# Performance work log

Hardware: AMD Instinct MI355X
Metric: run time of the kernel (lower is better)

Reference implementation:

```python
import jax, jax.numpy as jnp
import numpy as np

NIN = 1024
NOUT = 1024
NHEADS = 16
DHEAD = NOUT // NHEADS


def setup_inputs() -> dict:
    key = jax.random.key(0)
    k1, k2, k3, k4 = jax.random.split(key, 4)
    y = jax.random.normal(k1, (2, 2048, NIN), dtype=jnp.float32)
    Wqkv = jax.random.normal(k2, (NIN, 3 * NOUT), dtype=jnp.float32) * (1.0 / np.sqrt(NIN))
    Wff = jax.random.normal(k3, (NOUT, NOUT), dtype=jnp.float32) * (1.0 / np.sqrt(NOUT))
    bff = jax.random.normal(k4, (NOUT,), dtype=jnp.float32) * 0.01
    return {"y": y, "Wqkv": Wqkv, "Wff": Wff, "bff": bff}


def reference(y, Wqkv, Wff, bff):
    b, n, _ = y.shape
    qkv = y @ Wqkv  # [b, n, 3*nout]
    qkv = qkv.reshape(b, n, 3, NHEADS, DHEAD).transpose(2, 0, 3, 1, 4)
    q, k, v = qkv[0], qkv[1], qkv[2]  # each [b, h, n, d]
    att = jnp.einsum('bhqd,bhkd->bhqk', q, k)
    causal = jnp.triu(jnp.ones((n, n), dtype=bool), k=1)
    att = jnp.where(causal, -jnp.inf, att)
    att = jax.nn.softmax(att / jnp.sqrt(jnp.float32(DHEAD)), axis=-1)
    ctx = jnp.einsum('bhqk,bhkd->bhqd', att, v)
    ctx = ctx.transpose(0, 2, 1, 3).reshape(b, n, NOUT)
    return ctx @ Wff + bff
```

## Files before the change

kernel.cpp:

```cpp
#include <hip/hip_runtime.h>
#include <stdint.h>

#define NHEADS 16
#define DHEAD 64
#define SEQ 2048
#define BATCH 2
#define NINF 1024
#define NOUTF 1024
#define N3 3072
#define MTOT 4096

typedef unsigned short US;
typedef __attribute__((ext_vector_type(8))) short short8;
typedef __attribute__((ext_vector_type(4))) short short4v;
typedef __attribute__((ext_vector_type(4))) float f32x4;

__device__ inline US f2bf(float f) {
  union { float f; unsigned u; } v; v.f = f;
  unsigned r = v.u + 0x7fffu + ((v.u >> 16) & 1u);
  return (US)(r >> 16);
}

__device__ inline f32x4 mfma16(short8 a, short8 b, f32x4 c) {
  return __builtin_amdgcn_mfma_f32_16x16x32_bf16(a, b, c, 0, 0, 0);
}

__device__ inline f32x4 mfma16k16(short4v a, short4v b, f32x4 c) {
  return __builtin_amdgcn_mfma_f32_16x16x16bf16_1k(a, b, c, 0, 0, 0);
}

__device__ inline void async16(const US* g, US* l) {
  __builtin_amdgcn_global_load_lds(
      (const __attribute__((address_space(1))) unsigned int*)g,
      (__attribute__((address_space(3))) unsigned int*)l, 16, 0, 0);
}

__global__ __launch_bounds__(256) void k_pre(
    const float* __restrict__ y, US* __restrict__ ybf,
    const float* __restrict__ Wqkv, const float* __restrict__ Wff,
    US* __restrict__ dq, US* __restrict__ df) {
  __shared__ float tile[32][33];
  int bl = blockIdx.x;
  int tid = threadIdx.x;
  if (bl < 4096) {
    int i = bl * 256 + tid;
    float4 v = ((const float4*)y)[i];
    ushort4 o;
    o.x = f2bf(v.x); o.y = f2bf(v.y); o.z = f2bf(v.z); o.w = f2bf(v.w);
    ((ushort4*)ybf)[i] = o;
  } else {
    int bl2 = bl - 4096;
    int bxi = bl2 & 127, byi = bl2 >> 7;
    const float* src; US* dst; int C;
    if (bxi < 96) { src = Wqkv; dst = dq; C = N3; }
    else          { src = Wff;  dst = df; C = NOUTF; bxi -= 96; }
    int bx = bxi * 32, by = byi * 32;
    int tx = tid & 31, ty = tid >> 5;
    for (int i = 0; i < 32; i += 8)
      tile[ty + i][tx] = src[(size_t)(by + ty + i) * C + bx + tx];
    __syncthreads();
    for (int i = 0; i < 32; i += 8)
      dst[(size_t)(bx + ty + i) * 1024 + by + tx] = f2bf(tile[tx][ty + i]);
  }
}

__global__ void k_vtrans(const US* __restrict__ src, US* __restrict__ dst) {
  __shared__ US tile[32][33];
  int bh = blockIdx.z;
  int bx = blockIdx.x * 32;
  int by = blockIdx.y * 32;
  int tx = threadIdx.x, ty = threadIdx.y;
  const US* s0 = src + (size_t)bh * SEQ * DHEAD;
  US* d0 = dst + (size_t)bh * DHEAD * SEQ;
  for (int i = 0; i < 32; i += 8)
    tile[ty + i][tx] = s0[(size_t)(by + ty + i) * DHEAD + bx + tx];
  __syncthreads();
  for (int i = 0; i < 32; i += 8)
    d0[(size_t)(bx + ty + i) * SEQ + by + tx] = tile[tx][ty + i];
}

__global__ __launch_bounds__(256) void k_gemm_qkv(
    const US* __restrict__ A,
    const US* __restrict__ Bt,
    US* __restrict__ qbuf, US* __restrict__ kbuf, US* __restrict__ vbuf) {
  __shared__ US As[128 * 32];
  __shared__ US Bs[128 * 32];
  int tid = threadIdx.x;
  int wave = tid >> 6, lane = tid & 63, lm = lane & 15, lk = lane >> 4;
  int wm = wave >> 1, wn = wave & 1;
  int mbase = blockIdx.y * 128, nbase = blockIdx.x * 128;

  f32x4 acc[4][4];
#pragma unroll
  for (int i = 0; i < 4; ++i)
#pragma unroll
    for (int j = 0; j < 4; ++j) acc[i][j] = (f32x4){0.f, 0.f, 0.f, 0.f};

  const US* ga = A + (size_t)(mbase + (tid >> 2)) * NINF + (tid & 3) * 8;
  const US* gb = Bt + (size_t)(nbase + (tid >> 2)) * NINF + (tid & 3) * 8;
  US* la = As + tid * 8;
  US* lb = Bs + tid * 8;

  for (int kt = 0; kt < NINF / 32; ++kt) {
    int ko = kt * 32;
    async16(ga + ko, la);
    async16(ga + ko + (size_t)64 * NINF, la + 64 * 32);
    async16(gb + ko, lb);
    async16(gb + ko + (size_t)64 * NINF, lb + 64 * 32);
    __syncthreads();
    short8 a[4], b[4];
#pragma unroll
    for (int i = 0; i < 4; ++i)
      a[i] = *(const short8*)(As + (wm * 64 + i * 16 + lm) * 32 + lk * 8);
#pragma unroll
    for (int j = 0; j < 4; ++j)
      b[j] = *(const short8*)(Bs + (wn * 64 + j * 16 + lm) * 32 + lk * 8);
#pragma unroll
    for (int i = 0; i < 4; ++i)
#pragma unroll
      for (int j = 0; j < 4; ++j) acc[i][j] = mfma16(b[j], a[i], acc[i][j]);
    __syncthreads();
  }

  int which = nbase >> 10;
  US* dsts = (which == 0) ? qbuf : (which == 1) ? kbuf : vbuf;
  float sc = (which == 0) ? 0.18033688011112042f : 1.f;
  int hh = ((nbase + wn * 64) & 1023) >> 6;
#pragma unroll
  for (int i = 0; i < 4; ++i) {
    int row = mbase + wm * 64 + i * 16 + lm;
    int bh = (row >> 11) * NHEADS + hh;
    int s = row & (SEQ - 1);
    US* base = dsts + ((size_t)bh * SEQ + s) * DHEAD;
#pragma unroll
    for (int j = 0; j < 4; ++j) {
      int d0 = j * 16 + lk * 4;
      uint32_t lo = (uint32_t)f2bf(acc[i][j][0] * sc) | ((uint32_t)f2bf(acc[i][j][1] * sc) << 16);
      uint32_t hi = (uint32_t)f2bf(acc[i][j][2] * sc) | ((uint32_t)f2bf(acc[i][j][3] * sc) << 16);
      uint2 pv; pv.x = lo; pv.y = hi;
      *(uint2*)(base + d0) = pv;
    }
  }
}

__global__ __launch_bounds__(256) void k_attn(
    const US* __restrict__ qbuf, const US* __restrict__ kbuf,
    const US* __restrict__ vtbuf, US* __restrict__ ctx) {
  __shared__ US Ks[2][64 * 64];
  __shared__ US Vs[2][64 * 64];
  int tid = threadIdx.x;
  int w = tid >> 6, lane = tid & 63;
  int lm = lane & 15, lk = lane >> 4;
  int bl = blockIdx.x;
  int xcd = bl & 7, g = bl >> 3;
  int bh = (g & 3) * 8 + xcd;
  int q4 = g >> 2;
  int rnd = q4 >> 3, qq = q4 & 7;
  int s = (rnd == 0) ? 31 - qq : (rnd == 1) ? qq : (rnd == 2) ? 23 - qq : 8 + qq;
  int qb = s * 64 + w * 16;
  int nt = s + 1;

  const US* kbase = kbuf + (size_t)bh * SEQ * DHEAD;
  const US* vtb = vtbuf + (size_t)bh * DHEAD * SEQ;
  const US* qr = qbuf + ((size_t)bh * SEQ + qb + lm) * DHEAD + lk * 8;
  short8 qf0 = *(const short8*)(qr);
  short8 qf1 = *(const short8*)(qr + 32);

  int swz = ((lane & 7) ^ (lane >> 3)) * 8;
  const US* gsrc[4];
  US* ldst[4];
  int step[4];
#pragma unroll
  for (int j = 0; j < 4; ++j) {
    int u = w + 4 * j;
    if (u < 8) {
      gsrc[j] = kbase + (size_t)(u * 8 + (lane >> 3)) * DHEAD + swz;
      ldst[j] = &Ks[0][0] + u * 512 + lane * 8;
      step[j] = 64 * DHEAD;
    } else {
      int i = u - 8;
      gsrc[j] = vtb + (size_t)(i * 8 + (lane >> 3)) * SEQ + swz;
      ldst[j] = &Vs[0][0] + i * 512 + lane * 8;
      step[j] = 64;
    }
  }

  int xorv = lm & 7;
  int ck0 = ((lk) ^ xorv) * 16;
  int ck1 = ((4 + lk) ^ xorv) * 16;
  int cv[4];
#pragma unroll
  for (int kg = 0; kg < 4; ++kg)
    cv[kg] = (((kg * 2 + (lk >> 1)) ^ xorv) * 16) + (lk & 1) * 8;

  f32x4 o[4];
#pragma unroll
  for (int dg = 0; dg < 4; ++dg) o[dg] = (f32x4){0.f, 0.f, 0.f, 0.f};
  f32x4 lacc = (f32x4){0.f, 0.f, 0.f, 0.f};
  const short4v kones = {(short)0x3F80, (short)0x3F80, (short)0x3F80, (short)0x3F80};

  auto body = [&](const char* Kc, const char* Vc, int kg, bool dm) {
    const char* kr = Kc + (kg * 16 + lm) * 128;
    short8 ka0 = *(const short8*)(kr + ck0);
    short8 ka1 = *(const short8*)(kr + ck1);
    f32x4 st = (f32x4){0.f, 0.f, 0.f, 0.f};
    st = mfma16(ka0, qf0, st);
    st = mfma16(ka1, qf1, st);
    uint32_t ue[4];
#pragma unroll
    for (int r = 0; r < 4; ++r) {
      float v = st[r];
      if (dm && (lk * 4 + r > lm)) v = -INFINITY;
      union { float f; uint32_t u; } cv2;
      cv2.f = exp2f(v);
      ue[r] = cv2.u + 0x8000u;
    }
    union { short4v s4; uint32_t u[2]; } pk;
    pk.u[0] = __builtin_amdgcn_perm(ue[1], ue[0], 0x07060302u);
    pk.u[1] = __builtin_amdgcn_perm(ue[3], ue[2], 0x07060302u);
    lacc = mfma16k16(kones, pk.s4, lacc);
    const char* vr = Vc + lm * 128 + cv[kg];
#pragma unroll
    for (int dg = 0; dg < 4; ++dg) {
      short4v va = *(const short4v*)(vr + dg * 2048);
      o[dg] = mfma16k16(va, pk.s4, o[dg]);
    }
  };

#pragma unroll
  for (int j = 0; j < 4; ++j) { async16(gsrc[j], ldst[j]); gsrc[j] += step[j]; }
  if (nt > 1) {
#pragma unroll
    for (int j = 0; j < 4; ++j) { async16(gsrc[j], ldst[j] + 4096); gsrc[j] += step[j]; }
  }

  for (int t = 0; t < nt; ++t) {
    if (t + 1 < nt) asm volatile("s_waitcnt vmcnt(4)" ::: "memory");
    else            asm volatile("s_waitcnt vmcnt(0)" ::: "memory");
    __builtin_amdgcn_s_barrier();
    asm volatile("" ::: "memory");
    const char* Kc = (const char*)Ks + (t & 1) * 8192;
    const char* Vc = (const char*)Vs + (t & 1) * 8192;
    if (t < s) {
#pragma unroll
      for (int kg = 0; kg < 4; ++kg) body(Kc, Vc, kg, false);
    } else {
      for (int kg = 0; kg < w; ++kg) body(Kc, Vc, kg, false);
      body(Kc, Vc, w, true);
    }
    asm volatile("" ::: "memory");
    __builtin_amdgcn_s_barrier();
    asm volatile("" ::: "memory");
    if (t + 2 < nt) {
#pragma unroll
      for (int j = 0; j < 4; ++j) {
        async16(gsrc[j], ldst[j] + (t & 1) * 4096);
        gsrc[j] += step[j];
      }
    }
  }

  float inv = 1.f / lacc[0];

  US* crow = ctx + ((size_t)(bh >> 4) * SEQ + qb + lm) * NOUTF + (bh & 15) * DHEAD;
#pragma unroll
  for (int dg = 0; dg < 4; ++dg) {
    union { short4v s4; uint32_t u[2]; } pk;
    pk.u[0] = (uint32_t)f2bf(o[dg][0] * inv) | ((uint32_t)f2bf(o[dg][1] * inv) << 16);
    pk.u[1] = (uint32_t)f2bf(o[dg][2] * inv) | ((uint32_t)f2bf(o[dg][3] * inv) << 16);
    *(short4v*)(crow + dg * 16 + lk * 4) = pk.s4;
  }
}

__global__ __launch_bounds__(256) void k_gemm_out(
    const US* __restrict__ A, const US* __restrict__ Bt,
    const float* __restrict__ bias, float* __restrict__ out) {
  __shared__ US As[64 * 32];
  __shared__ US Bs[64 * 32];
  int tid = threadIdx.x;
  int wave = tid >> 6, lane = tid & 63, lm = lane & 15, lk = lane >> 4;
  int wm = wave >> 1, wn = wave & 1;
  int mbase = blockIdx.y * 64, nbase = blockIdx.x * 64;

  f32x4 acc[2][2];
#pragma unroll
  for (int i = 0; i < 2; ++i)
#pragma unroll
    for (int j = 0; j < 2; ++j) acc[i][j] = (f32x4){0.f, 0.f, 0.f, 0.f};

  const US* ga = A + (size_t)(mbase + (tid >> 2)) * NOUTF + (tid & 3) * 8;
  const US* gb = Bt + (size_t)(nbase + (tid >> 2)) * NOUTF + (tid & 3) * 8;
  US* la = As + tid * 8;
  US* lb = Bs + tid * 8;

  for (int kt = 0; kt < NOUTF / 32; ++kt) {
    int ko = kt * 32;
    async16(ga + ko, la);
    async16(gb + ko, lb);
    __syncthreads();
    short8 a[2], b[2];
#pragma unroll
    for (int i = 0; i < 2; ++i)
      a[i] = *(const short8*)(As + (wm * 32 + i * 16 + lm) * 32 + lk * 8);
#pragma unroll
    for (int j = 0; j < 2; ++j)
      b[j] = *(const short8*)(Bs + (wn * 32 + j * 16 + lm) * 32 + lk * 8);
#pragma unroll
    for (int i = 0; i < 2; ++i)
#pragma unroll
      for (int j = 0; j < 2; ++j) acc[i][j] = mfma16(b[j], a[i], acc[i][j]);
    __syncthreads();
  }

#pragma unroll
  for (int j = 0; j < 2; ++j) {
    int n0 = nbase + wn * 32 + j * 16 + lk * 4;
    float4 bv = *(const float4*)(bias + n0);
#pragma unroll
    for (int i = 0; i < 2; ++i) {
      int row = mbase + wm * 32 + i * 16 + lm;
      float4 ov;
      ov.x = acc[i][j][0] + bv.x;
      ov.y = acc[i][j][1] + bv.y;
      ov.z = acc[i][j][2] + bv.z;
      ov.w = acc[i][j][3] + bv.w;
      *(float4*)(out + (size_t)row * NOUTF + n0) = ov;
    }
  }
}

extern "C" void kernel_launch(void* const* d_in, const int* in_sizes, int n_in,
                              void* d_out, int out_size, void* d_ws, size_t ws_size,
                              hipStream_t stream) {
  const float* y    = (const float*)d_in[0];
  const float* Wqkv = (const float*)d_in[1];
  const float* Wff  = (const float*)d_in[2];
  const float* bff  = (const float*)d_in[3];
  float* out = (float*)d_out;

  char* ws = (char*)d_ws;
  US* ybf   = (US*)(ws);
  US* ctx   = (US*)(ws);
  US* wqkvt = (US*)(ws + (8u << 20));
  US* wfft  = (US*)(ws + (14u << 20));
  US* qbuf  = (US*)(ws + (16u << 20));
  US* kbuf  = (US*)(ws + (24u << 20));
  US* vbuf  = (US*)(ws + (32u << 20));
  US* vtbuf = (US*)(ws + (40u << 20));

  k_pre<<<dim3(8192), 256, 0, stream>>>(y, ybf, Wqkv, Wff, wqkvt, wfft);
  k_gemm_qkv<<<dim3(N3 / 128, MTOT / 128), 256, 0, stream>>>(ybf, wqkvt, qbuf, kbuf, vbuf);
  k_vtrans<<<dim3(DHEAD / 32, SEQ / 32, BATCH * NHEADS), dim3(32, 8), 0, stream>>>(vbuf, vtbuf);
  k_attn<<<dim3(1024), 256, 0, stream>>>(qbuf, kbuf, vtbuf, ctx);
  k_gemm_out<<<dim3(NOUTF / 64, MTOT / 64), 256, 0, stream>>>(ctx, wfft, bff, out);
}
```

Measured before the change: 183.0 us.

## Deepen QKV GEMM K-tile with XOR-swizzled LDS and enlarge output GEMM tile

The QKV GEMM now stages a 64-wide K slice per iteration instead of 32, halving the barrier count, and places the data with an XOR swizzle on 16-byte chunks to avoid LDS bank conflicts. The output GEMM moves from 64x64 to 128x64 block tiles, with each wave covering 32 rows and all 64 columns, and swaps the MFMA operand order so its epilogue writes scalar floats along columns. The larger tiles raise data reuse per LDS load but double shared memory and accumulator registers, which can lower occupancy. The new scalar stores in the output epilogue may also be less efficient than the earlier float4 stores.

```diff
diff --git a/kernel.cpp b/kernel.cpp
--- a/kernel.cpp
+++ b/kernel.cpp
@@ -83,8 +83,8 @@
     const US* __restrict__ A,
     const US* __restrict__ Bt,
     US* __restrict__ qbuf, US* __restrict__ kbuf, US* __restrict__ vbuf) {
-  __shared__ US As[128 * 32];
-  __shared__ US Bs[128 * 32];
+  __shared__ US As[128 * 64];
+  __shared__ US Bs[128 * 64];
   int tid = threadIdx.x;
   int wave = tid >> 6, lane = tid & 63, lm = lane & 15, lk = lane >> 4;
   int wm = wave >> 1, wn = wave & 1;
@@ -96,29 +96,41 @@
 #pragma unroll
     for (int j = 0; j < 4; ++j) acc[i][j] = (f32x4){0.f, 0.f, 0.f, 0.f};
 
-  const US* ga = A + (size_t)(mbase + (tid >> 2)) * NINF + (tid & 3) * 8;
-  const US* gb = Bt + (size_t)(nbase + (tid >> 2)) * NINF + (tid & 3) * 8;
+  int ru = tid >> 3;
+  int su = (tid & 7) ^ (ru & 7);
+  const US* ga = A + (size_t)(mbase + ru) * NINF + su * 8;
+  const US* gb = Bt + (size_t)(nbase + ru) * NINF + su * 8;
   US* la = As + tid * 8;
   US* lb = Bs + tid * 8;
 
-  for (int kt = 0; kt < NINF / 32; ++kt) {
-    int ko = kt * 32;
-    async16(ga + ko, la);
-    async16(ga + ko + (size_t)64 * NINF, la + 64 * 32);
-    async16(gb + ko, lb);
-    async16(gb + ko + (size_t)64 * NINF, lb + 64 * 32);
-    __syncthreads();
-    short8 a[4], b[4];
-#pragma unroll
-    for (int i = 0; i < 4; ++i)
-      a[i] = *(const short8*)(As + (wm * 64 + i * 16 + lm) * 32 + lk * 8);
-#pragma unroll
-    for (int j = 0; j < 4; ++j)
-      b[j] = *(const short8*)(Bs + (wn * 64 + j * 16 + lm) * 32 + lk * 8);
-#pragma unroll
-    for (int i = 0; i < 4; ++i)
-#pragma unroll
-      for (int j = 0; j < 4; ++j) acc[i][j] = mfma16(b[j], a[i], acc[i][j]);
+  int xorv = lm & 7;
+
+  for (int kt = 0; kt < 16; ++kt) {
+    int ko = kt * 64;
+#pragma unroll
+    for (int p = 0; p < 4; ++p) {
+      async16(ga + ko + (size_t)(p * 32) * NINF, la + p * 2048);
+      async16(gb + ko + (size_t)(p * 32) * NINF, lb + p * 2048);
+    }
+    __syncthreads();
+    short8 a[2][4], b[2][4];
+#pragma unroll
+    for (int kk = 0; kk < 2; ++kk) {
+      int u = (kk * 4 + lk) ^ xorv;
+#pragma unroll
+      for (int i = 0; i < 4; ++i)
+        a[kk][i] = *(const short8*)(As + (wm * 64 + i * 16 + lm) * 64 + u * 8);
+#pragma unroll
+      for (int j = 0; j < 4; ++j)
+        b[kk][j] = *(const short8*)(Bs + (wn * 64 + j * 16 + lm) * 64 + u * 8);
+    }
+#pragma unroll
+    for (int kk = 0; kk < 2; ++kk)
+#pragma unroll
+      for (int i = 0; i < 4; ++i)
+#pragma unroll
+        for (int j = 0; j < 4; ++j)
+          acc[i][j] = mfma16(b[kk][j], a[kk][i], acc[i][j]);
     __syncthreads();
   }
 
@@ -275,18 +287,17 @@
 __global__ __launch_bounds__(256) void k_gemm_out(
     const US* __restrict__ A, const US* __restrict__ Bt,
     const float* __restrict__ bias, float* __restrict__ out) {
-  __shared__ US As[64 * 32];
+  __shared__ US As[128 * 32];
   __shared__ US Bs[64 * 32];
   int tid = threadIdx.x;
   int wave = tid >> 6, lane = tid & 63, lm = lane & 15, lk = lane >> 4;
-  int wm = wave >> 1, wn = wave & 1;
-  int mbase = blockIdx.y * 64, nbase = blockIdx.x * 64;
-
-  f32x4 acc[2][2];
+  int mbase = blockIdx.y * 128, nbase = blockIdx.x * 64;
+
+  f32x4 acc[2][4];
 #pragma unroll
   for (int i = 0; i < 2; ++i)
 #pragma unroll
-    for (int j = 0; j < 2; ++j) acc[i][j] = (f32x4){0.f, 0.f, 0.f, 0.f};
+    for (int j = 0; j < 4; ++j) acc[i][j] = (f32x4){0.f, 0.f, 0.f, 0.f};
 
   const US* ga = A + (size_t)(mbase + (tid >> 2)) * NOUTF + (tid & 3) * 8;
   const US* gb = Bt + (size_t)(nbase + (tid >> 2)) * NOUTF + (tid & 3) * 8;
@@ -296,36 +307,34 @@
   for (int kt = 0; kt < NOUTF / 32; ++kt) {
     int ko = kt * 32;
     async16(ga + ko, la);
+    async16(ga + ko + (size_t)64 * NOUTF, la + 64 * 32);
     async16(gb + ko, lb);
     __syncthreads();
-    short8 a[2], b[2];
+    short8 a[2], b[4];
 #pragma unroll
     for (int i = 0; i < 2; ++i)
-      a[i] = *(const short8*)(As + (wm * 32 + i * 16 + lm) * 32 + lk * 8);
-#pragma unroll
-    for (int j = 0; j < 2; ++j)
-      b[j] = *(const short8*)(Bs + (wn * 32 + j * 16 + lm) * 32 + lk * 8);
+      a[i] = *(const short8*)(As + (wave * 32 + i * 16 + lm) * 32 + lk * 8);
+#pragma unroll
+    for (int j = 0; j < 4; ++j)
+      b[j] = *(const short8*)(Bs + (j * 16 + lm) * 32 + lk * 8);
 #pragma unroll
     for (int i = 0; i < 2; ++i)
 #pragma unroll
-      for (int j = 0; j < 2; ++j) acc[i][j] = mfma16(b[j], a[i], acc[i][j]);
-    __syncthreads();
-  }
-
-#pragma unroll
-  for (int j = 0; j < 2; ++j) {
-    int n0 = nbase + wn * 32 + j * 16 + lk * 4;
-    float4 bv = *(const float4*)(bias + n0);
-#pragma unroll
-    for (int i = 0; i < 2; ++i) {
-      int row = mbase + wm * 32 + i * 16 + lm;
-      float4 ov;
-      ov.x = acc[i][j][0] + bv.x;
-      ov.y = acc[i][j][1] + bv.y;
-      ov.z = acc[i][j][2] + bv.z;
-      ov.w = acc[i][j][3] + bv.w;
-      *(float4*)(out + (size_t)row * NOUTF + n0) = ov;
-    }
+      for (int j = 0; j < 4; ++j) acc[i][j] = mfma16(a[i], b[j], acc[i][j]);
+    __syncthreads();
+  }
+
+#pragma unroll
+  for (int j = 0; j < 4; ++j) {
+    int col = nbase + j * 16 + lm;
+    float bv = bias[col];
+#pragma unroll
+    for (int i = 0; i < 2; ++i)
+#pragma unroll
+      for (int r = 0; r < 4; ++r) {
+        int row = mbase + wave * 32 + i * 16 + lk * 4 + r;
+        out[(size_t)row * NOUTF + col] = acc[i][j][r] + bv;
+      }
   }
 }
 
@@ -352,5 +361,5 @@
   k_gemm_qkv<<<dim3(N3 / 128, MTOT / 128), 256, 0, stream>>>(ybf, wqkvt, qbuf, kbuf, vbuf);
   k_vtrans<<<dim3(DHEAD / 32, SEQ / 32, BATCH * NHEADS), dim3(32, 8), 0, stream>>>(vbuf, vtbuf);
   k_attn<<<dim3(1024), 256, 0, stream>>>(qbuf, kbuf, vtbuf, ctx);
-  k_gemm_out<<<dim3(NOUTF / 64, MTOT / 64), 256, 0, stream>>>(ctx, wfft, bff, out);
-}
+  k_gemm_out<<<dim3(NOUTF / 64, MTOT / 128), 256, 0, stream>>>(ctx, wfft, bff, out);
+}
```

Measured after the change: 194.1 us. +6.1%, slower.

## Fuse all stages into one persistent kernel with software grid barriers

Applied to the files above, without the earlier changes.

Replaces the five separate kernel launches with a single persistent kernel of 1024 blocks. The stages (convert/transpose, QKV GEMM, V transpose, attention, output GEMM) are separated by atomic-counter grid barriers, and the counter lives in the first word of the output buffer, zeroed by a memset. The aim is to remove kernel launch gaps and tail idling between stages. In exchange, correctness depends on all 1024 blocks being co-resident (launch bounds 256,4). The QKV GEMM also uses only 768 of the blocks, and the spin barriers add their own overhead.

```diff
diff --git a/kernel.cpp b/kernel.cpp
--- a/kernel.cpp
+++ b/kernel.cpp
@@ -9,6 +9,7 @@
 #define NOUTF 1024
 #define N3 3072
 #define MTOT 4096
+#define MB (1u << 20)
 
 typedef unsigned short US;
 typedef __attribute__((ext_vector_type(8))) short short8;
@@ -35,296 +36,320 @@
       (__attribute__((address_space(3))) unsigned int*)l, 16, 0, 0);
 }
 
-__global__ __launch_bounds__(256) void k_pre(
-    const float* __restrict__ y, US* __restrict__ ybf,
-    const float* __restrict__ Wqkv, const float* __restrict__ Wff,
-    US* __restrict__ dq, US* __restrict__ df) {
-  __shared__ float tile[32][33];
+__device__ inline void gbar(unsigned* cnt, unsigned th) {
+  __syncthreads();
+  if (threadIdx.x == 0) {
+    __threadfence();
+    atomicAdd(cnt, 1u);
+    while (__hip_atomic_load(cnt, __ATOMIC_RELAXED, __HIP_MEMORY_SCOPE_AGENT) < th)
+      __builtin_amdgcn_s_sleep(2);
+    __threadfence();
+  }
+  __syncthreads();
+}
+
+__global__ __launch_bounds__(256, 4) void k_fused(
+    const float* __restrict__ y, const float* __restrict__ Wqkv,
+    const float* __restrict__ Wff, const float* __restrict__ bff,
+    float* __restrict__ out, char* __restrict__ ws) {
+  __shared__ __align__(16) char smem[32768];
+  US* ybf   = (US*)(ws);
+  US* ctx   = (US*)(ws);
+  US* wqkvt = (US*)(ws + 8 * MB);
+  US* wfft  = (US*)(ws + 14 * MB);
+  US* qbuf  = (US*)(ws + 16 * MB);
+  US* kbuf  = (US*)(ws + 24 * MB);
+  US* vbuf  = (US*)(ws + 32 * MB);
+  US* vtbuf = (US*)(ws + 40 * MB);
+  unsigned* cnt = (unsigned*)out;
   int bl = blockIdx.x;
   int tid = threadIdx.x;
-  if (bl < 4096) {
-    int i = bl * 256 + tid;
-    float4 v = ((const float4*)y)[i];
-    ushort4 o;
-    o.x = f2bf(v.x); o.y = f2bf(v.y); o.z = f2bf(v.z); o.w = f2bf(v.w);
-    ((ushort4*)ybf)[i] = o;
-  } else {
-    int bl2 = bl - 4096;
-    int bxi = bl2 & 127, byi = bl2 >> 7;
-    const float* src; US* dst; int C;
-    if (bxi < 96) { src = Wqkv; dst = dq; C = N3; }
-    else          { src = Wff;  dst = df; C = NOUTF; bxi -= 96; }
-    int bx = bxi * 32, by = byi * 32;
+  int wave = tid >> 6, lane = tid & 63, lm = lane & 15, lk = lane >> 4;
+
+  {
+#pragma unroll
+    for (int p = 0; p < 4; ++p) {
+      int i = (p * 1024 + bl) * 256 + tid;
+      float4 v = ((const float4*)y)[i];
+      ushort4 o;
+      o.x = f2bf(v.x); o.y = f2bf(v.y); o.z = f2bf(v.z); o.w = f2bf(v.w);
+      ((ushort4*)ybf)[i] = o;
+    }
+    float (*tile)[33] = (float(*)[33])smem;
     int tx = tid & 31, ty = tid >> 5;
-    for (int i = 0; i < 32; i += 8)
-      tile[ty + i][tx] = src[(size_t)(by + ty + i) * C + bx + tx];
-    __syncthreads();
-    for (int i = 0; i < 32; i += 8)
-      dst[(size_t)(bx + ty + i) * 1024 + by + tx] = f2bf(tile[tx][ty + i]);
-  }
-}
-
-__global__ void k_vtrans(const US* __restrict__ src, US* __restrict__ dst) {
-  __shared__ US tile[32][33];
-  int bh = blockIdx.z;
-  int bx = blockIdx.x * 32;
-  int by = blockIdx.y * 32;
-  int tx = threadIdx.x, ty = threadIdx.y;
-  const US* s0 = src + (size_t)bh * SEQ * DHEAD;
-  US* d0 = dst + (size_t)bh * DHEAD * SEQ;
-  for (int i = 0; i < 32; i += 8)
-    tile[ty + i][tx] = s0[(size_t)(by + ty + i) * DHEAD + bx + tx];
-  __syncthreads();
-  for (int i = 0; i < 32; i += 8)
-    d0[(size_t)(bx + ty + i) * SEQ + by + tx] = tile[tx][ty + i];
-}
-
-__global__ __launch_bounds__(256) void k_gemm_qkv(
-    const US* __restrict__ A,
-    const US* __restrict__ Bt,
-    US* __restrict__ qbuf, US* __restrict__ kbuf, US* __restrict__ vbuf) {
-  __shared__ US As[128 * 32];
-  __shared__ US Bs[128 * 32];
-  int tid = threadIdx.x;
-  int wave = tid >> 6, lane = tid & 63, lm = lane & 15, lk = lane >> 4;
-  int wm = wave >> 1, wn = wave & 1;
-  int mbase = blockIdx.y * 128, nbase = blockIdx.x * 128;
-
-  f32x4 acc[4][4];
-#pragma unroll
-  for (int i = 0; i < 4; ++i)
-#pragma unroll
-    for (int j = 0; j < 4; ++j) acc[i][j] = (f32x4){0.f, 0.f, 0.f, 0.f};
-
-  const US* ga = A + (size_t)(mbase + (tid >> 2)) * NINF + (tid & 3) * 8;
-  const US* gb = Bt + (size_t)(nbase + (tid >> 2)) * NINF + (tid & 3) * 8;
-  US* la = As + tid * 8;
-  US* lb = Bs + tid * 8;
-
-  for (int kt = 0; kt < NINF / 32; ++kt) {
-    int ko = kt * 32;
-    async16(ga + ko, la);
-    async16(ga + ko + (size_t)64 * NINF, la + 64 * 32);
-    async16(gb + ko, lb);
-    async16(gb + ko + (size_t)64 * NINF, lb + 64 * 32);
-    __syncthreads();
-    short8 a[4], b[4];
+    for (int q = 0; q < 4; ++q) {
+      int t = bl * 4 + q;
+      int bxi = t & 127, byi = t >> 7;
+      const float* src; US* dst; int C;
+      if (bxi < 96) { src = Wqkv; dst = wqkvt; C = N3; }
+      else          { src = Wff;  dst = wfft;  C = NOUTF; bxi -= 96; }
+      int bx = bxi * 32, by = byi * 32;
+      for (int i2 = 0; i2 < 32; i2 += 8)
+        tile[ty + i2][tx] = src[(size_t)(by + ty + i2) * C + bx + tx];
+      __syncthreads();
+      for (int i2 = 0; i2 < 32; i2 += 8)
+        dst[(size_t)(bx + ty + i2) * 1024 + by + tx] = f2bf(tile[tx][ty + i2]);
+      __syncthreads();
+    }
+  }
+  gbar(cnt, 1024u);
+
+  if (bl < 768) {
+    US* As = (US*)smem;
+    US* Bs = (US*)(smem + 8192);
+    int wm = wave >> 1, wn = wave & 1;
+    int mbase = (bl / 24) * 128, nbase = (bl % 24) * 128;
+
+    f32x4 acc[4][4];
 #pragma unroll
     for (int i = 0; i < 4; ++i)
-      a[i] = *(const short8*)(As + (wm * 64 + i * 16 + lm) * 32 + lk * 8);
-#pragma unroll
-    for (int j = 0; j < 4; ++j)
-      b[j] = *(const short8*)(Bs + (wn * 64 + j * 16 + lm) * 32 + lk * 8);
-#pragma unroll
-    for (int i = 0; i < 4; ++i)
-#pragma unroll
-      for (int j = 0; j < 4; ++j) acc[i][j] = mfma16(b[j], a[i], acc[i][j]);
-    __syncthreads();
-  }
-
-  int which = nbase >> 10;
-  US* dsts = (which == 0) ? qbuf : (which == 1) ? kbuf : vbuf;
-  float sc = (which == 0) ? 0.18033688011112042f : 1.f;
-  int hh = ((nbase + wn * 64) & 1023) >> 6;
-#pragma unroll
-  for (int i = 0; i < 4; ++i) {
-    int row = mbase + wm * 64 + i * 16 + lm;
-    int bh = (row >> 11) * NHEADS + hh;
-    int s = row & (SEQ - 1);
-    US* base = dsts + ((size_t)bh * SEQ + s) * DHEAD;
+#pragma unroll
+      for (int j = 0; j < 4; ++j) acc[i][j] = (f32x4){0.f, 0.f, 0.f, 0.f};
+
+    const US* ga = ybf + (size_t)(mbase + (tid >> 2)) * NINF + (tid & 3) * 8;
+    const US* gb = wqkvt + (size_t)(nbase + (tid >> 2)) * NINF + (tid & 3) * 8;
+    US* la = As + tid * 8;
+    US* lb = Bs + tid * 8;
+
+    for (int kt = 0; kt < 32; ++kt) {
+      int ko = kt * 32;
+      async16(ga + ko, la);
+      async16(ga + ko + (size_t)64 * NINF, la + 2048);
+      async16(gb + ko, lb);
+      async16(gb + ko + (size_t)64 * NINF, lb + 2048);
+      __syncthreads();
+      short8 a[4], b[4];
+#pragma unroll
+      for (int i = 0; i < 4; ++i)
+        a[i] = *(const short8*)(As + (wm * 64 + i * 16 + lm) * 32 + lk * 8);
+#pragma unroll
+      for (int j = 0; j < 4; ++j)
+        b[j] = *(const short8*)(Bs + (wn * 64 + j * 16 + lm) * 32 + lk * 8);
+#pragma unroll
+      for (int i = 0; i < 4; ++i)
+#pragma unroll
+        for (int j = 0; j < 4; ++j) acc[i][j] = mfma16(b[j], a[i], acc[i][j]);
+      __syncthreads();
+    }
+
+    int which = nbase >> 10;
+    US* dsts = (which == 0) ? qbuf : (which == 1) ? kbuf : vbuf;
+    float sc = (which == 0) ? 0.18033688011112042f : 1.f;
+    int hh = ((nbase + wn * 64) & 1023) >> 6;
+#pragma unroll
+    for (int i = 0; i < 4; ++i) {
+      int row = mbase + wm * 64 + i * 16 + lm;
+      int bh = (row >> 11) * NHEADS + hh;
+      int s = row & (SEQ - 1);
+      US* base = dsts + ((size_t)bh * SEQ + s) * DHEAD;
+#pragma unroll
+      for (int j = 0; j < 4; ++j) {
+        int d0 = j * 16 + lk * 4;
+        uint32_t lo = (uint32_t)f2bf(acc[i][j][0] * sc) | ((uint32_t)f2bf(acc[i][j][1] * sc) << 16);
+        uint32_t hi = (uint32_t)f2bf(acc[i][j][2] * sc) | ((uint32_t)f2bf(acc[i][j][3] * sc) << 16);
+        uint2 pv; pv.x = lo; pv.y = hi;
+        *(uint2*)(base + d0) = pv;
+      }
+    }
+  }
+  gbar(cnt, 2048u);
+
+  {
+    US (*tile)[33] = (US(*)[33])smem;
+    int tx = tid & 31, ty = tid >> 5;
+#pragma unroll
+    for (int q = 0; q < 4; ++q) {
+      int t = q * 1024 + bl;
+      int bh = t & 31;
+      int sy = (t >> 5) & 63;
+      int dx = t >> 11;
+      const US* s0 = vbuf + (size_t)bh * SEQ * DHEAD;
+      US* d0 = vtbuf + (size_t)bh * DHEAD * SEQ;
+      int bx = dx * 32, by = sy * 32;
+      for (int i2 = 0; i2 < 32; i2 += 8)
+        tile[ty + i2][tx] = s0[(size_t)(by + ty + i2) * DHEAD + bx + tx];
+      __syncthreads();
+      for (int i2 = 0; i2 < 32; i2 += 8)
+        d0[(size_t)(bx + ty + i2) * SEQ + by + tx] = tile[tx][ty + i2];
+      __syncthreads();
+    }
+  }
+  gbar(cnt, 3072u);
+
+  {
+    US* KsP = (US*)smem;
+    US* VsP = (US*)(smem + 16384);
+    int w = wave;
+    int xcd = bl & 7, g = bl >> 3;
+    int bh = (g & 3) * 8 + xcd;
+    int q4 = g >> 2;
+    int rnd = q4 >> 3, qq = q4 & 7;
+    int s = (rnd == 0) ? 31 - qq : (rnd == 1) ? qq : (rnd == 2) ? 23 - qq : 8 + qq;
+    int qb = s * 64 + w * 16;
+    int nt = s + 1;
+
+    const US* kbase = kbuf + (size_t)bh * SEQ * DHEAD;
+    const US* vtb = vtbuf + (size_t)bh * DHEAD * SEQ;
+    const US* qr = qbuf + ((size_t)bh * SEQ + qb + lm) * DHEAD + lk * 8;
+    short8 qf0 = *(const short8*)(qr);
+    short8 qf1 = *(const short8*)(qr + 32);
+
+    int swz = ((lane & 7) ^ (lane >> 3)) * 8;
+    const US* gsrc[4];
+    US* ldst[4];
+    int step[4];
 #pragma unroll
     for (int j = 0; j < 4; ++j) {
-      int d0 = j * 16 + lk * 4;
-      uint32_t lo = (uint32_t)f2bf(acc[i][j][0] * sc) | ((uint32_t)f2bf(acc[i][j][1] * sc) << 16);
-      uint32_t hi = (uint32_t)f2bf(acc[i][j][2] * sc) | ((uint32_t)f2bf(acc[i][j][3] * sc) << 16);
-      uint2 pv; pv.x = lo; pv.y = hi;
-      *(uint2*)(base + d0) = pv;
-    }
-  }
-}
-
-__global__ __launch_bounds__(256) void k_attn(
-    const US* __restrict__ qbuf, const US* __restrict__ kbuf,
-    const US* __restrict__ vtbuf, US* __restrict__ ctx) {
-  __shared__ US Ks[2][64 * 64];
-  __shared__ US Vs[2][64 * 64];
-  int tid = threadIdx.x;
-  int w = tid >> 6, lane = tid & 63;
-  int lm = lane & 15, lk = lane >> 4;
-  int bl = blockIdx.x;
-  int xcd = bl & 7, g = bl >> 3;
-  int bh = (g & 3) * 8 + xcd;
-  int q4 = g >> 2;
-  int rnd = q4 >> 3, qq = q4 & 7;
-  int s = (rnd == 0) ? 31 - qq : (rnd == 1) ? qq : (rnd == 2) ? 23 - qq : 8 + qq;
-  int qb = s * 64 + w * 16;
-  int nt = s + 1;
-
-  const US* kbase = kbuf + (size_t)bh * SEQ * DHEAD;
-  const US* vtb = vtbuf + (size_t)bh * DHEAD * SEQ;
-  const US* qr = qbuf + ((size_t)bh * SEQ + qb + lm) * DHEAD + lk * 8;
-  short8 qf0 = *(const short8*)(qr);
-  short8 qf1 = *(const short8*)(qr + 32);
-
-  int swz = ((lane & 7) ^ (lane >> 3)) * 8;
-  const US* gsrc[4];
-  US* ldst[4];
-  int step[4];
-#pragma unroll
-  for (int j = 0; j < 4; ++j) {
-    int u = w + 4 * j;
-    if (u < 8) {
-      gsrc[j] = kbase + (size_t)(u * 8 + (lane >> 3)) * DHEAD + swz;
-      ldst[j] = &Ks[0][0] + u * 512 + lane * 8;
-      step[j] = 64 * DHEAD;
-    } else {
-      int i = u - 8;
-      gsrc[j] = vtb + (size_t)(i * 8 + (lane >> 3)) * SEQ + swz;
-      ldst[j] = &Vs[0][0] + i * 512 + lane * 8;
-      step[j] = 64;
-    }
-  }
-
-  int xorv = lm & 7;
-  int ck0 = ((lk) ^ xorv) * 16;
-  int ck1 = ((4 + lk) ^ xorv) * 16;
-  int cv[4];
-#pragma unroll
-  for (int kg = 0; kg < 4; ++kg)
-    cv[kg] = (((kg * 2 + (lk >> 1)) ^ xorv) * 16) + (lk & 1) * 8;
-
-  f32x4 o[4];
-#pragma unroll
-  for (int dg = 0; dg < 4; ++dg) o[dg] = (f32x4){0.f, 0.f, 0.f, 0.f};
-  f32x4 lacc = (f32x4){0.f, 0.f, 0.f, 0.f};
-  const short4v kones = {(short)0x3F80, (short)0x3F80, (short)0x3F80, (short)0x3F80};
-
-  auto body = [&](const char* Kc, const char* Vc, int kg, bool dm) {
-    const char* kr = Kc + (kg * 16 + lm) * 128;
-    short8 ka0 = *(const short8*)(kr + ck0);
-    short8 ka1 = *(const short8*)(kr + ck1);
-    f32x4 st = (f32x4){0.f, 0.f, 0.f, 0.f};
-    st = mfma16(ka0, qf0, st);
-    st = mfma16(ka1, qf1, st);
-    uint32_t ue[4];
-#pragma unroll
-    for (int r = 0; r < 4; ++r) {
-      float v = st[r];
-      if (dm && (lk * 4 + r > lm)) v = -INFINITY;
-      union { float f; uint32_t u; } cv2;
-      cv2.f = exp2f(v);
-      ue[r] = cv2.u + 0x8000u;
-    }
-    union { short4v s4; uint32_t u[2]; } pk;
-    pk.u[0] = __builtin_amdgcn_perm(ue[1], ue[0], 0x07060302u);
-    pk.u[1] = __builtin_amdgcn_perm(ue[3], ue[2], 0x07060302u);
-    lacc = mfma16k16(kones, pk.s4, lacc);
-    const char* vr = Vc + lm * 128 + cv[kg];
+      int u = w + 4 * j;
+      if (u < 8) {
+        gsrc[j] = kbase + (size_t)(u * 8 + (lane >> 3)) * DHEAD + swz;
+        ldst[j] = KsP + u * 512 + lane * 8;
+        step[j] = 64 * DHEAD;
+      } else {
+        int i = u - 8;
+        gsrc[j] = vtb + (size_t)(i * 8 + (lane >> 3)) * SEQ + swz;
+        ldst[j] = VsP + i * 512 + lane * 8;
+        step[j] = 64;
+      }
+    }
+
+    int xorv = lm & 7;
+    int ck0 = ((lk) ^ xorv) * 16;
+    int ck1 = ((4 + lk) ^ xorv) * 16;
+    int cv[4];
+#pragma unroll
+    for (int kg = 0; kg < 4; ++kg)
+      cv[kg] = (((kg * 2 + (lk >> 1)) ^ xorv) * 16) + (lk & 1) * 8;
+
+    f32x4 o[4];
+#pragma unroll
+    for (int dg = 0; dg < 4; ++dg) o[dg] = (f32x4){0.f, 0.f, 0.f, 0.f};
+    f32x4 lacc = (f32x4){0.f, 0.f, 0.f, 0.f};
+    const short4v kones = {(short)0x3F80, (short)0x3F80, (short)0x3F80, (short)0x3F80};
+
+    auto body = [&](const char* Kc, const char* Vc, int kg, bool dm) {
+      const char* kr = Kc + (kg * 16 + lm) * 128;
+      short8 ka0 = *(const short8*)(kr + ck0);
+      short8 ka1 = *(const short8*)(kr + ck1);
+      f32x4 st = (f32x4){0.f, 0.f, 0.f, 0.f};
+      st = mfma16(ka0, qf0, st);
+      st = mfma16(ka1, qf1, st);
+      uint32_t ue[4];
+#pragma unroll
+      for (int r = 0; r < 4; ++r) {
+        float v = st[r];
+        if (dm && (lk * 4 + r > lm)) v = -INFINITY;
+        union { float f; uint32_t u; } cv2;
+        cv2.f = exp2f(v);
+        ue[r] = cv2.u + 0x8000u;
+      }
+      union { short4v s4; uint32_t u[2]; } pk;
+      pk.u[0] = __builtin_amdgcn_perm(ue[1], ue[0], 0x07060302u);
+      pk.u[1] = __builtin_amdgcn_perm(ue[3], ue[2], 0x07060302u);
+      lacc = mfma16k16(kones, pk.s4, lacc);
+      const char* vr = Vc + lm * 128 + cv[kg];
+#pragma unroll
+      for (int dg = 0; dg < 4; ++dg) {
+        short4v va = *(const short4v*)(vr + dg * 2048);
+        o[dg] = mfma16k16(va, pk.s4, o[dg]);
+      }
+    };
+
+#pragma unroll
+    for (int j = 0; j < 4; ++j) { async16(gsrc[j], ldst[j]); gsrc[j] += step[j]; }
+    if (nt > 1) {
+#pragma unroll
+      for (int j = 0; j < 4; ++j) { async16(gsrc[j], ldst[j] + 4096); gsrc[j] += step[j]; }
+    }
+
+    for (int t = 0; t < nt; ++t) {
+      if (t + 1 < nt) asm volatile("s_waitcnt vmcnt(4)" ::: "memory");
+      else            asm volatile("s_waitcnt vmcnt(0)" ::: "memory");
+      __builtin_amdgcn_s_barrier();
+      asm volatile("" ::: "memory");
+      const char* Kc = (const char*)KsP + (t & 1) * 8192;
+      const char* Vc = (const char*)VsP + (t & 1) * 8192;
+      if (t < s) {
+#pragma unroll
+        for (int kg = 0; kg < 4; ++kg) body(Kc, Vc, kg, false);
+      } else {
+        for (int kg = 0; kg < w; ++kg) body(Kc, Vc, kg, false);
+        body(Kc, Vc, w, true);
+      }
+      asm volatile("" ::: "memory");
+      __builtin_amdgcn_s_barrier();
+      asm volatile("" ::: "memory");
+      if (t + 2 < nt) {
+#pragma unroll
+        for (int j = 0; j < 4; ++j) {
+          async16(gsrc[j], ldst[j] + (t & 1) * 4096);
+          gsrc[j] += step[j];
+        }
+      }
+    }
+
+    float inv = 1.f / lacc[0];
+    US* crow = ctx + ((size_t)(bh >> 4) * SEQ + qb + lm) * NOUTF + (bh & 15) * DHEAD;
 #pragma unroll
     for (int dg = 0; dg < 4; ++dg) {
-      short4v va = *(const short4v*)(vr + dg * 2048);
-      o[dg] = mfma16k16(va, pk.s4, o[dg]);
-    }
-  };
-
-#pragma unroll
-  for (int j = 0; j < 4; ++j) { async16(gsrc[j], ldst[j]); gsrc[j] += step[j]; }
-  if (nt > 1) {
-#pragma unroll
-    for (int j = 0; j < 4; ++j) { async16(gsrc[j], ldst[j] + 4096); gsrc[j] += step[j]; }
-  }
-
-  for (int t = 0; t < nt; ++t) {
-    if (t + 1 < nt) asm volatile("s_waitcnt vmcnt(4)" ::: "memory");
-    else            asm volatile("s_waitcnt vmcnt(0)" ::: "memory");
-    __builtin_amdgcn_s_barrier();
-    asm volatile("" ::: "memory");
-    const char* Kc = (const char*)Ks + (t & 1) * 8192;
-    const char* Vc = (const char*)Vs + (t & 1) * 8192;
-    if (t < s) {
-#pragma unroll
-      for (int kg = 0; kg < 4; ++kg) body(Kc, Vc, kg, false);
-    } else {
-      for (int kg = 0; kg < w; ++kg) body(Kc, Vc, kg, false);
-      body(Kc, Vc, w, true);
-    }
-    asm volatile("" ::: "memory");
-    __builtin_amdgcn_s_barrier();
-    asm volatile("" ::: "memory");
-    if (t + 2 < nt) {
-#pragma unroll
-      for (int j = 0; j < 4; ++j) {
-        async16(gsrc[j], ldst[j] + (t & 1) * 4096);
-        gsrc[j] += step[j];
-      }
-    }
-  }
-
-  float inv = 1.f / lacc[0];
-
-  US* crow = ctx + ((size_t)(bh >> 4) * SEQ + qb + lm) * NOUTF + (bh & 15) * DHEAD;
-#pragma unroll
-  for (int dg = 0; dg < 4; ++dg) {
-    union { short4v s4; uint32_t u[2]; } pk;
-    pk.u[0] = (uint32_t)f2bf(o[dg][0] * inv) | ((uint32_t)f2bf(o[dg][1] * inv) << 16);
-    pk.u[1] = (uint32_t)f2bf(o[dg][2] * inv) | ((uint32_t)f2bf(o[dg][3] * inv) << 16);
-    *(short4v*)(crow + dg * 16 + lk * 4) = pk.s4;
-  }
-}
-
-__global__ __launch_bounds__(256) void k_gemm_out(
-    const US* __restrict__ A, const US* __restrict__ Bt,
-    const float* __restrict__ bias, float* __restrict__ out) {
-  __shared__ US As[64 * 32];
-  __shared__ US Bs[64 * 32];
-  int tid = threadIdx.x;
-  int wave = tid >> 6, lane = tid & 63, lm = lane & 15, lk = lane >> 4;
-  int wm = wave >> 1, wn = wave & 1;
-  int mbase = blockIdx.y * 64, nbase = blockIdx.x * 64;
-
-  f32x4 acc[2][2];
-#pragma unroll
-  for (int i = 0; i < 2; ++i)
-#pragma unroll
-    for (int j = 0; j < 2; ++j) acc[i][j] = (f32x4){0.f, 0.f, 0.f, 0.f};
-
-  const US* ga = A + (size_t)(mbase + (tid >> 2)) * NOUTF + (tid & 3) * 8;
-  const US* gb = Bt + (size_t)(nbase + (tid >> 2)) * NOUTF + (tid & 3) * 8;
-  US* la = As + tid * 8;
-  US* lb = Bs + tid * 8;
-
-  for (int kt = 0; kt < NOUTF / 32; ++kt) {
-    int ko = kt * 32;
-    async16(ga + ko, la);
-    async16(gb + ko, lb);
-    __syncthreads();
-    short8 a[2], b[2];
+      union { short4v s4; uint32_t u[2]; } pk;
+      pk.u[0] = (uint32_t)f2bf(o[dg][0] * inv) | ((uint32_t)f2bf(o[dg][1] * inv) << 16);
+      pk.u[1] = (uint32_t)f2bf(o[dg][2] * inv) | ((uint32_t)f2bf(o[dg][3] * inv) << 16);
+      *(short4v*)(crow + dg * 16 + lk * 4) = pk.s4;
+    }
+  }
+  gbar(cnt, 4096u);
+
+  {
+    US* As = (US*)smem;
+    US* Bs = (US*)(smem + 4096);
+    int wm = wave >> 1, wn = wave & 1;
+    int mbase = (bl >> 4) * 64, nbase = (bl & 15) * 64;
+
+    f32x4 acc[2][2];
 #pragma unroll
     for (int i = 0; i < 2; ++i)
-      a[i] = *(const short8*)(As + (wm * 32 + i * 16 + lm) * 32 + lk * 8);
-#pragma unroll
-    for (int j = 0; j < 2; ++j)
-      b[j] = *(const short8*)(Bs + (wn * 32 + j * 16 + lm) * 32 + lk * 8);
-#pragma unroll
-    for (int i = 0; i < 2; ++i)
-#pragma unroll
-      for (int j = 0; j < 2; ++j) acc[i][j] = mfma16(b[j], a[i], acc[i][j]);
-    __syncthreads();
-  }
-
-#pragma unroll
-  for (int j = 0; j < 2; ++j) {
-    int n0 = nbase + wn * 32 + j * 16 + lk * 4;
-    float4 bv = *(const float4*)(bias + n0);
-#pragma unroll
-    for (int i = 0; i < 2; ++i) {
-      int row = mbase + wm * 32 + i * 16 + lm;
-      float4 ov;
-      ov.x = acc[i][j][0] + bv.x;
-      ov.y = acc[i][j][1] + bv.y;
-      ov.z = acc[i][j][2] + bv.z;
-      ov.w = acc[i][j][3] + bv.w;
-      *(float4*)(out + (size_t)row * NOUTF + n0) = ov;
+#pragma unroll
+      for (int j = 0; j < 2; ++j) acc[i][j] = (f32x4){0.f, 0.f, 0.f, 0.f};
+
+    const US* ga = ctx + (size_t)(mbase + (tid >> 2)) * NOUTF + (tid & 3) * 8;
+    const US* gb = wfft + (size_t)(nbase + (tid >> 2)) * NOUTF + (tid & 3) * 8;
+    US* la = As + tid * 8;
+    US* lb = Bs + tid * 8;
+
+    for (int kt = 0; kt < 32; ++kt) {
+      int ko = kt * 32;
+      async16(ga + ko, la);
+      async16(gb + ko, lb);
+      __syncthreads();
+      short8 a[2], b[2];
+#pragma unroll
+      for (int i = 0; i < 2; ++i)
+        a[i] = *(const short8*)(As + (wm * 32 + i * 16 + lm) * 32 + lk * 8);
+#pragma unroll
+      for (int j = 0; j < 2; ++j)
+        b[j] = *(const short8*)(Bs + (wn * 32 + j * 16 + lm) * 32 + lk * 8);
+#pragma unroll
+      for (int i = 0; i < 2; ++i)
+#pragma unroll
+        for (int j = 0; j < 2; ++j) acc[i][j] = mfma16(b[j], a[i], acc[i][j]);
+      __syncthreads();
+    }
+
+#pragma unroll
+    for (int j = 0; j < 2; ++j) {
+      int n0 = nbase + wn * 32 + j * 16 + lk * 4;
+      float4 bv = *(const float4*)(bff + n0);
+#pragma unroll
+      for (int i = 0; i < 2; ++i) {
+        int row = mbase + wm * 32 + i * 16 + lm;
+        float4 ov;
+        ov.x = acc[i][j][0] + bv.x;
+        ov.y = acc[i][j][1] + bv.y;
+        ov.z = acc[i][j][2] + bv.z;
+        ov.w = acc[i][j][3] + bv.w;
+        *(float4*)(out + (size_t)row * NOUTF + n0) = ov;
+      }
     }
   }
 }
@@ -338,19 +363,6 @@
   const float* bff  = (const float*)d_in[3];
   float* out = (float*)d_out;
 
-  char* ws = (char*)d_ws;
-  US* ybf   = (US*)(ws);
-  US* ctx   = (US*)(ws);
-  US* wqkvt = (US*)(ws + (8u << 20));
-  US* wfft  = (US*)(ws + (14u << 20));
-  US* qbuf  = (US*)(ws + (16u << 20));
-  US* kbuf  = (US*)(ws + (24u << 20));
-  US* vbuf  = (US*)(ws + (32u << 20));
-  US* vtbuf = (US*)(ws + (40u << 20));
-
-  k_pre<<<dim3(8192), 256, 0, stream>>>(y, ybf, Wqkv, Wff, wqkvt, wfft);
-  k_gemm_qkv<<<dim3(N3 / 128, MTOT / 128), 256, 0, stream>>>(ybf, wqkvt, qbuf, kbuf, vbuf);
-  k_vtrans<<<dim3(DHEAD / 32, SEQ / 32, BATCH * NHEADS), dim3(32, 8), 0, stream>>>(vbuf, vtbuf);
-  k_attn<<<dim3(1024), 256, 0, stream>>>(qbuf, kbuf, vtbuf, ctx);
-  k_gemm_out<<<dim3(NOUTF / 64, MTOT / 64), 256, 0, stream>>>(ctx, wfft, bff, out);
-}
+  hipMemsetAsync(d_out, 0, 4, stream);
+  k_fused<<<dim3(1024), 256, 0, stream>>>(y, Wqkv, Wff, bff, out, (char*)d_ws);
+}
```

After: 640.3 us. +249.9%, slower.
